# Optimization experiments

Measured on AMD Instinct MI355X. Metric: run time of the kernel, lower is better.

The kernel has to match this reference:

```python
import jax, jax.numpy as jnp
import numpy as np

D_MODEL = 1024
D_PROJ = D_MODEL // 4


def setup_inputs() -> dict:
    key = jax.random.key(0)
    k1, k2, k3 = jax.random.split(key, 3)
    hidden_states = jax.random.normal(k1, (4, 2048, D_MODEL), dtype=jnp.float32)
    proj_w = jax.random.normal(k2, (D_PROJ, D_MODEL), dtype=jnp.float32) * 0.02
    proj_b = jnp.zeros((D_PROJ,), dtype=jnp.float32)
    clf_w = jax.random.normal(k3, (1, 1), dtype=jnp.float32) * 0.02
    clf_b = jnp.zeros((1,), dtype=jnp.float32)
    return {"hidden_states": hidden_states, "proj_w": proj_w, "proj_b": proj_b,
            "clf_w": clf_w, "clf_b": clf_b}


def reference(hidden_states, proj_w, proj_b, clf_w, clf_b):
    # h: [B, S, D/4]
    h = jax.nn.relu(jnp.einsum('bsd,pd->bsp', hidden_states, proj_w) + proj_b)
    # pairwise dot products == batched h @ h^T: [B, S, S]
    scores = jnp.einsum('bip,bjp->bij', h, h)
    # scalar affine classifier (Linear(1,1)) folded in
    return scores * clf_w[0, 0] + clf_b[0]
```

## Files before the change

### kernel.cpp

```cpp
#include <hip/hip_runtime.h>
#include <hip/hip_bf16.h>

typedef __bf16 bf16_t;
typedef __attribute__((ext_vector_type(8))) __bf16 bf16x8;
typedef __attribute__((ext_vector_type(4))) float f32x4;

#define SEQ    2048
#define DMODEL 1024
#define DPROJ  256
#define NBATCH 4

__device__ __forceinline__ bf16x8 cvt8(const float4& lo, const float4& hi) {
    bf16x8 v;
    v[0] = (bf16_t)lo.x; v[1] = (bf16_t)lo.y; v[2] = (bf16_t)lo.z; v[3] = (bf16_t)lo.w;
    v[4] = (bf16_t)hi.x; v[5] = (bf16_t)hi.y; v[6] = (bf16_t)hi.z; v[7] = (bf16_t)hi.w;
    return v;
}

__global__ __launch_bounds__(256) void proj_kernel(
    const float* __restrict__ X, const float* __restrict__ W,
    const float* __restrict__ bias, bf16_t* __restrict__ H)
{
    __shared__ __align__(16) bf16_t Xs[64 * 64];
    __shared__ __align__(16) bf16_t Ws[64 * 64];

    const int m0 = blockIdx.x * 64;
    const int n0 = blockIdx.y * 64;
    const int tid  = threadIdx.x;
    const int lane = tid & 63;
    const int wave = tid >> 6;
    const int quad = lane >> 4;
    const int l16  = lane & 15;
    const int wm = (wave & 1) * 32;
    const int wn = (wave >> 1) * 32;
    const int swz = l16 & 7;

    int srow[2], scol[2];
    bf16_t* lx[2];
    bf16_t* lw[2];
    #pragma unroll
    for (int r = 0; r < 2; ++r) {
        const int p = r * 256 + tid;
        srow[r] = p >> 3;
        scol[r] = p & 7;
        const int cs = (scol[r] ^ (srow[r] & 7)) * 8;
        lx[r] = Xs + srow[r] * 64 + cs;
        lw[r] = Ws + srow[r] * 64 + cs;
    }

    float4 xr[2][2][2], wr[2][2][2];

    #pragma unroll
    for (int s = 0; s < 2; ++s) {
        const int k0 = s * 64;
        #pragma unroll
        for (int r = 0; r < 2; ++r) {
            const float* gx = X + (size_t)(m0 + srow[r]) * DMODEL + k0 + scol[r] * 8;
            xr[s][r][0] = *(const float4*)gx;
            xr[s][r][1] = *(const float4*)(gx + 4);
            const float* gw = W + (size_t)(n0 + srow[r]) * DMODEL + k0 + scol[r] * 8;
            wr[s][r][0] = *(const float4*)gw;
            wr[s][r][1] = *(const float4*)(gw + 4);
        }
    }

    f32x4 acc[2][2] = {};

    #pragma unroll
    for (int kt = 0; kt < 16; ++kt) {
        const int s = kt & 1;
        __syncthreads();
        #pragma unroll
        for (int r = 0; r < 2; ++r) {
            *(bf16x8*)lx[r] = cvt8(xr[s][r][0], xr[s][r][1]);
            *(bf16x8*)lw[r] = cvt8(wr[s][r][0], wr[s][r][1]);
        }
        __syncthreads();

        if (kt < 14) {
            const int k0 = (kt + 2) * 64;
            #pragma unroll
            for (int r = 0; r < 2; ++r) {
                const float* gx = X + (size_t)(m0 + srow[r]) * DMODEL + k0 + scol[r] * 8;
                xr[s][r][0] = *(const float4*)gx;
                xr[s][r][1] = *(const float4*)(gx + 4);
                const float* gw = W + (size_t)(n0 + srow[r]) * DMODEL + k0 + scol[r] * 8;
                wr[s][r][0] = *(const float4*)gw;
                wr[s][r][1] = *(const float4*)(gw + 4);
            }
        }

        #pragma unroll
        for (int ks = 0; ks < 2; ++ks) {
            bf16x8 af[2], bfr[2];
            #pragma unroll
            for (int i = 0; i < 2; ++i) {
                const int ch = (((ks << 2) | quad) ^ swz) * 8;
                af[i]  = *(const bf16x8*)&Xs[(wm + i * 16 + l16) * 64 + ch];
                bfr[i] = *(const bf16x8*)&Ws[(wn + i * 16 + l16) * 64 + ch];
            }
            #pragma unroll
            for (int i = 0; i < 2; ++i)
                #pragma unroll
                for (int j = 0; j < 2; ++j)
                    acc[i][j] = __builtin_amdgcn_mfma_f32_16x16x32_bf16(
                        af[i], bfr[j], acc[i][j], 0, 0, 0);
        }
    }

    #pragma unroll
    for (int i = 0; i < 2; ++i) {
        #pragma unroll
        for (int j = 0; j < 2; ++j) {
            const int gn = n0 + wn + j * 16 + l16;
            const float bv = bias[gn];
            #pragma unroll
            for (int r = 0; r < 4; ++r) {
                const int gm = m0 + wm + i * 16 + quad * 4 + r;
                float v = acc[i][j][r] + bv;
                v = v > 0.f ? v : 0.f;
                H[(size_t)gm * DPROJ + gn] = (bf16_t)v;
            }
        }
    }
}

__global__ __launch_bounds__(256, 2) void score_kernel(
    const bf16_t* __restrict__ H, const float* __restrict__ clf_w,
    const float* __restrict__ clf_b, float* __restrict__ Out)
{
    int t = blockIdx.x, bi = 0, rl = SEQ / 128;
    while (t >= rl) { t -= rl; --rl; ++bi; }
    const int bj = bi + t;
    const int b  = blockIdx.y;
    const int m0 = bi * 128;
    const int n0 = bj * 128;
    const bf16_t* Hb = H + (size_t)b * SEQ * DPROJ;
    float* Ob = Out + (size_t)b * SEQ * SEQ;

    const int tid  = threadIdx.x;
    const int lane = tid & 63;
    const int wave = tid >> 6;
    const int quad = lane >> 4;
    const int l16  = lane & 15;
    const int wm = (wave & 1) * 64;
    const int wn = (wave >> 1) * 64;

    const bf16_t* pa = Hb + (size_t)(m0 + wm + l16) * DPROJ + quad * 8;
    const bf16_t* pb = Hb + (size_t)(n0 + wn + l16) * DPROJ + quad * 8;

    f32x4 acc[4][4] = {};

    #pragma unroll
    for (int ks = 0; ks < 8; ++ks) {
        bf16x8 af[4], bfr[4];
        #pragma unroll
        for (int i = 0; i < 4; ++i) {
            af[i]  = *(const bf16x8*)(pa + (size_t)(i * 16) * DPROJ + ks * 32);
            bfr[i] = *(const bf16x8*)(pb + (size_t)(i * 16) * DPROJ + ks * 32);
        }
        #pragma unroll
        for (int i = 0; i < 4; ++i)
            #pragma unroll
            for (int j = 0; j < 4; ++j)
                acc[i][j] = __builtin_amdgcn_mfma_f32_16x16x32_bf16(
                    af[i], bfr[j], acc[i][j], 0, 0, 0);
    }

    const float scale = clf_w[0];
    const float off   = clf_b[0];

    #pragma unroll
    for (int i = 0; i < 4; ++i) {
        #pragma unroll
        for (int r = 0; r < 4; ++r) {
            const int gm = m0 + wm + i * 16 + quad * 4 + r;
            float* row = Ob + (size_t)gm * SEQ + n0 + wn + l16;
            #pragma unroll
            for (int j = 0; j < 4; ++j)
                row[j * 16] = acc[i][j][r] * scale + off;
        }
    }

    if (bi != bj) {
        #pragma unroll
        for (int j = 0; j < 4; ++j) {
            const int gn = n0 + wn + j * 16 + l16;
            float* row = Ob + (size_t)gn * SEQ + m0 + wm + quad * 4;
            #pragma unroll
            for (int i = 0; i < 4; ++i) {
                float4 v;
                v.x = acc[i][j][0] * scale + off;
                v.y = acc[i][j][1] * scale + off;
                v.z = acc[i][j][2] * scale + off;
                v.w = acc[i][j][3] * scale + off;
                *(float4*)(row + i * 16) = v;
            }
        }
    }
}

extern "C" void kernel_launch(void* const* d_in, const int* in_sizes, int n_in,
                              void* d_out, int out_size, void* d_ws, size_t ws_size,
                              hipStream_t stream) {
    const float* X    = (const float*)d_in[0];
    const float* W    = (const float*)d_in[1];
    const float* bias = (const float*)d_in[2];
    const float* clfw = (const float*)d_in[3];
    const float* clfb = (const float*)d_in[4];
    float* Out = (float*)d_out;
    bf16_t* H  = (bf16_t*)d_ws;

    dim3 g1(NBATCH * SEQ / 64, DPROJ / 64, 1);
    proj_kernel<<<g1, 256, 0, stream>>>(X, W, bias, H);

    const int ntile = SEQ / 128;
    dim3 g2(ntile * (ntile + 1) / 2, NBATCH);
    score_kernel<<<g2, 256, 0, stream>>>(H, clfw, clfb, Out);
}
```

Baseline: 131.8 us.

## Stage score tiles through LDS with direct global-to-LDS loads and smaller tiles

```diff
diff --git a/kernel.cpp b/kernel.cpp
--- a/kernel.cpp
+++ b/kernel.cpp
@@ -17,15 +17,21 @@
     return v;
 }
 
+__device__ __forceinline__ void gl_lds16(const void* g, void* l) {
+    __builtin_amdgcn_global_load_lds(
+        (const __attribute__((address_space(1))) unsigned int*)g,
+        (__attribute__((address_space(3))) unsigned int*)l, 16, 0, 0);
+}
+
 __global__ __launch_bounds__(256) void proj_kernel(
     const float* __restrict__ X, const float* __restrict__ W,
     const float* __restrict__ bias, bf16_t* __restrict__ H)
 {
-    __shared__ __align__(16) bf16_t Xs[64 * 64];
-    __shared__ __align__(16) bf16_t Ws[64 * 64];
-
-    const int m0 = blockIdx.x * 64;
-    const int n0 = blockIdx.y * 64;
+    __shared__ __align__(16) bf16_t Xs[64 * 128];
+    __shared__ __align__(16) bf16_t Ws[64 * 128];
+
+    const int m0 = (blockIdx.x >> 2) * 64;
+    const int n0 = (blockIdx.x & 3) * 64;
     const int tid  = threadIdx.x;
     const int lane = tid & 63;
     const int wave = tid >> 6;
@@ -35,26 +41,22 @@
     const int wn = (wave >> 1) * 32;
     const int swz = l16 & 7;
 
-    int srow[2], scol[2];
-    bf16_t* lx[2];
-    bf16_t* lw[2];
-    #pragma unroll
-    for (int r = 0; r < 2; ++r) {
+    int srow[4], scol[4], soff[4];
+    #pragma unroll
+    for (int r = 0; r < 4; ++r) {
         const int p = r * 256 + tid;
-        srow[r] = p >> 3;
-        scol[r] = p & 7;
-        const int cs = (scol[r] ^ (srow[r] & 7)) * 8;
-        lx[r] = Xs + srow[r] * 64 + cs;
-        lw[r] = Ws + srow[r] * 64 + cs;
-    }
-
-    float4 xr[2][2][2], wr[2][2][2];
+        srow[r] = p >> 4;
+        scol[r] = p & 15;
+        soff[r] = srow[r] * 128 + ((scol[r] ^ (srow[r] & 7)) * 8);
+    }
+
+    float4 xr[2][4][2], wr[2][4][2];
 
     #pragma unroll
     for (int s = 0; s < 2; ++s) {
-        const int k0 = s * 64;
-        #pragma unroll
-        for (int r = 0; r < 2; ++r) {
+        const int k0 = s * 128;
+        #pragma unroll
+        for (int r = 0; r < 4; ++r) {
             const float* gx = X + (size_t)(m0 + srow[r]) * DMODEL + k0 + scol[r] * 8;
             xr[s][r][0] = *(const float4*)gx;
             xr[s][r][1] = *(const float4*)(gx + 4);
@@ -67,20 +69,20 @@
     f32x4 acc[2][2] = {};
 
     #pragma unroll
-    for (int kt = 0; kt < 16; ++kt) {
+    for (int kt = 0; kt < 8; ++kt) {
         const int s = kt & 1;
         __syncthreads();
         #pragma unroll
-        for (int r = 0; r < 2; ++r) {
-            *(bf16x8*)lx[r] = cvt8(xr[s][r][0], xr[s][r][1]);
-            *(bf16x8*)lw[r] = cvt8(wr[s][r][0], wr[s][r][1]);
-        }
-        __syncthreads();
-
-        if (kt < 14) {
-            const int k0 = (kt + 2) * 64;
-            #pragma unroll
-            for (int r = 0; r < 2; ++r) {
+        for (int r = 0; r < 4; ++r) {
+            *(bf16x8*)&Xs[soff[r]] = cvt8(xr[s][r][0], xr[s][r][1]);
+            *(bf16x8*)&Ws[soff[r]] = cvt8(wr[s][r][0], wr[s][r][1]);
+        }
+        __syncthreads();
+
+        if (kt < 6) {
+            const int k0 = (kt + 2) * 128;
+            #pragma unroll
+            for (int r = 0; r < 4; ++r) {
                 const float* gx = X + (size_t)(m0 + srow[r]) * DMODEL + k0 + scol[r] * 8;
                 xr[s][r][0] = *(const float4*)gx;
                 xr[s][r][1] = *(const float4*)(gx + 4);
@@ -91,13 +93,13 @@
         }
 
         #pragma unroll
-        for (int ks = 0; ks < 2; ++ks) {
+        for (int ks = 0; ks < 4; ++ks) {
             bf16x8 af[2], bfr[2];
+            const int ch = (((ks << 2) | quad) ^ swz) * 8;
             #pragma unroll
             for (int i = 0; i < 2; ++i) {
-                const int ch = (((ks << 2) | quad) ^ swz) * 8;
-                af[i]  = *(const bf16x8*)&Xs[(wm + i * 16 + l16) * 64 + ch];
-                bfr[i] = *(const bf16x8*)&Ws[(wn + i * 16 + l16) * 64 + ch];
+                af[i]  = *(const bf16x8*)&Xs[(wm + i * 16 + l16) * 128 + ch];
+                bfr[i] = *(const bf16x8*)&Ws[(wn + i * 16 + l16) * 128 + ch];
             }
             #pragma unroll
             for (int i = 0; i < 2; ++i)
@@ -125,16 +127,19 @@
     }
 }
 
-__global__ __launch_bounds__(256, 2) void score_kernel(
+__global__ __launch_bounds__(256, 8) void score_kernel(
     const bf16_t* __restrict__ H, const float* __restrict__ clf_w,
     const float* __restrict__ clf_b, float* __restrict__ Out)
 {
-    int t = blockIdx.x, bi = 0, rl = SEQ / 128;
+    __shared__ __align__(16) bf16_t As[64 * 64];
+    __shared__ __align__(16) bf16_t Bs[64 * 64];
+
+    int t = blockIdx.x, bi = 0, rl = SEQ / 64;
     while (t >= rl) { t -= rl; --rl; ++bi; }
     const int bj = bi + t;
     const int b  = blockIdx.y;
-    const int m0 = bi * 128;
-    const int n0 = bj * 128;
+    const int m0 = bi * 64;
+    const int n0 = bj * 64;
     const bf16_t* Hb = H + (size_t)b * SEQ * DPROJ;
     float* Ob = Out + (size_t)b * SEQ * SEQ;
 
@@ -143,60 +148,84 @@
     const int wave = tid >> 6;
     const int quad = lane >> 4;
     const int l16  = lane & 15;
-    const int wm = (wave & 1) * 64;
-    const int wn = (wave >> 1) * 64;
-
-    const bf16_t* pa = Hb + (size_t)(m0 + wm + l16) * DPROJ + quad * 8;
-    const bf16_t* pb = Hb + (size_t)(n0 + wn + l16) * DPROJ + quad * 8;
-
-    f32x4 acc[4][4] = {};
-
-    #pragma unroll
-    for (int ks = 0; ks < 8; ++ks) {
-        bf16x8 af[4], bfr[4];
-        #pragma unroll
-        for (int i = 0; i < 4; ++i) {
-            af[i]  = *(const bf16x8*)(pa + (size_t)(i * 16) * DPROJ + ks * 32);
-            bfr[i] = *(const bf16x8*)(pb + (size_t)(i * 16) * DPROJ + ks * 32);
-        }
-        #pragma unroll
-        for (int i = 0; i < 4; ++i)
-            #pragma unroll
-            for (int j = 0; j < 4; ++j)
-                acc[i][j] = __builtin_amdgcn_mfma_f32_16x16x32_bf16(
-                    af[i], bfr[j], acc[i][j], 0, 0, 0);
+    const int wm = (wave & 1) * 32;
+    const int wn = (wave >> 1) * 32;
+    const int swz = l16 & 7;
+
+    const bf16_t* gA[2];
+    const bf16_t* gB[2];
+    bf16_t* lA[2];
+    bf16_t* lB[2];
+    #pragma unroll
+    for (int t2 = 0; t2 < 2; ++t2) {
+        const int g   = (wave * 2 + t2) * 64 + lane;
+        const int row = g >> 3;
+        const int gc  = (g & 7) ^ (row & 7);
+        gA[t2] = Hb + (size_t)(m0 + row) * DPROJ + gc * 8;
+        gB[t2] = Hb + (size_t)(n0 + row) * DPROJ + gc * 8;
+        lA[t2] = As + (wave * 2 + t2) * 512;
+        lB[t2] = Bs + (wave * 2 + t2) * 512;
+    }
+
+    f32x4 acc[2][2] = {};
+
+    for (int kt = 0; kt < 4; ++kt) {
+        __syncthreads();
+        #pragma unroll
+        for (int t2 = 0; t2 < 2; ++t2) {
+            gl_lds16(gA[t2], lA[t2]);
+            gl_lds16(gB[t2], lB[t2]);
+        }
+        __syncthreads();
+        #pragma unroll
+        for (int t2 = 0; t2 < 2; ++t2) { gA[t2] += 64; gB[t2] += 64; }
+
+        #pragma unroll
+        for (int ks = 0; ks < 2; ++ks) {
+            const int ch = (((ks << 2) | quad) ^ swz) * 8;
+            bf16x8 af[2], bfr[2];
+            #pragma unroll
+            for (int i = 0; i < 2; ++i) {
+                af[i]  = *(const bf16x8*)&As[(wm + i * 16 + l16) * 64 + ch];
+                bfr[i] = *(const bf16x8*)&Bs[(wn + i * 16 + l16) * 64 + ch];
+            }
+            #pragma unroll
+            for (int i = 0; i < 2; ++i)
+                #pragma unroll
+                for (int j = 0; j < 2; ++j)
+                    acc[i][j] = __builtin_amdgcn_mfma_f32_16x16x32_bf16(
+                        af[i], bfr[j], acc[i][j], 0, 0, 0);
+        }
     }
 
     const float scale = clf_w[0];
     const float off   = clf_b[0];
 
     #pragma unroll
-    for (int i = 0; i < 4; ++i) {
-        #pragma unroll
-        for (int r = 0; r < 4; ++r) {
-            const int gm = m0 + wm + i * 16 + quad * 4 + r;
-            float* row = Ob + (size_t)gm * SEQ + n0 + wn + l16;
-            #pragma unroll
-            for (int j = 0; j < 4; ++j)
-                row[j * 16] = acc[i][j][r] * scale + off;
-        }
-    }
+    for (int i = 0; i < 2; ++i)
+        #pragma unroll
+        for (int j = 0; j < 2; ++j)
+            #pragma unroll
+            for (int r = 0; r < 4; ++r) {
+                const int gm = m0 + wm + i * 16 + quad * 4 + r;
+                const int gn = n0 + wn + j * 16 + l16;
+                Ob[(size_t)gm * SEQ + gn] = acc[i][j][r] * scale + off;
+            }
 
     if (bi != bj) {
         #pragma unroll
-        for (int j = 0; j < 4; ++j) {
-            const int gn = n0 + wn + j * 16 + l16;
-            float* row = Ob + (size_t)gn * SEQ + m0 + wm + quad * 4;
-            #pragma unroll
-            for (int i = 0; i < 4; ++i) {
+        for (int i = 0; i < 2; ++i)
+            #pragma unroll
+            for (int j = 0; j < 2; ++j) {
+                const int gn = n0 + wn + j * 16 + l16;
+                const int gm = m0 + wm + i * 16 + quad * 4;
                 float4 v;
                 v.x = acc[i][j][0] * scale + off;
                 v.y = acc[i][j][1] * scale + off;
                 v.z = acc[i][j][2] * scale + off;
                 v.w = acc[i][j][3] * scale + off;
-                *(float4*)(row + i * 16) = v;
-            }
-        }
+                *(float4*)&Ob[(size_t)gn * SEQ + gm] = v;
+            }
     }
 }
 
@@ -211,10 +240,10 @@
     float* Out = (float*)d_out;
     bf16_t* H  = (bf16_t*)d_ws;
 
-    dim3 g1(NBATCH * SEQ / 64, DPROJ / 64, 1);
+    dim3 g1(NBATCH * SEQ / 64 * (DPROJ / 64), 1, 1);
     proj_kernel<<<g1, 256, 0, stream>>>(X, W, bias, H);
 
-    const int ntile = SEQ / 128;
+    const int ntile = SEQ / 64;
     dim3 g2(ntile * (ntile + 1) / 2, NBATCH);
     score_kernel<<<g2, 256, 0, stream>>>(H, clfw, clfb, Out);
 }
```

Result: no change. 130.5 us (-1.0%).
